# Kernel tuning notes

Measured on AMD Instinct MI355X. Metric: run time of the kernel, lower is better.

## Reference

```python
import jax, jax.numpy as jnp
import numpy as np

C, H, N, B, L = 1, 512, 64, 16, 2048  # n_channels, n_heads, d_kernel, batch, seq_len


def setup_inputs() -> dict:
    key = jax.random.key(0)
    k1, k2 = jax.random.split(key)
    u = jax.random.normal(k1, (B, C * H, L), dtype=jnp.float32)
    k = jax.random.normal(k2, (C, H, N), dtype=jnp.float32)
    return {"u": u, "k": k}


def _l1_normalize(x, axis):
    # torch.linalg.norm(x, ord=1, dim=axis, keepdim=True): vector 1-norm along `axis`
    return x / jnp.sum(jnp.abs(x), axis=axis, keepdims=True)


def _forward(u, k):
    c, h, n = k.shape
    bsz, d, l = u.shape  # d == c*h
    dt = u.dtype
    # Shift matrix A: A[:, :, 1:, :-1] = I  (companion-style shift)
    A = jnp.zeros((c, h, n, n), dtype=dt).at[:, :, 1:, :-1].set(jnp.eye(n - 1, dtype=dt))
    # b = e1 broadcast to (c, h, n)
    b_vec = jnp.zeros((c, h, n), dtype=dt).at[:, :, 0].set(1.0)
    # closed-loop: k_norm = L1-normalize(clamp(k, 1/16, 1)); A_cl = L1-normalize(A + b k^T)
    k_norm = _l1_normalize(jnp.clip(k, 1.0 / 16.0, 1.0), axis=2)
    BK = jnp.einsum('chi,chj->chij', b_vec, k_norm)
    M = _l1_normalize(A + BK, axis=2)

    # Krylov recurrence: f[i] = k . (M^i b), i = 0..l-1
    def step(x, _):
        f_i = jnp.einsum('chn,chn->ch', k, x)
        x_next = jnp.einsum('chij,chj->chi', M, x)
        return x_next, f_i

    _, f = jax.lax.scan(step, b_vec, None, length=l)  # f: (l, c, h)
    f = jnp.moveaxis(f, 0, -1)  # (c, h, l)

    # Causal FFT convolution of u (b, c, h, l) with filter f (c, h, l)
    n_fft = 2 * l
    uf = jnp.fft.rfft(u.reshape(bsz, c, h, l), n=n_fft)
    ff = jnp.fft.rfft(f, n=n_fft)
    y = jnp.fft.irfft(uf * ff[None], n=n_fft)[..., :l]
    return y.reshape(bsz, c * h, l)


def reference(u, k):
    return _forward(u, k)
```

## Files before the change

kernel.cpp:

```cpp
#include <hip/hip_runtime.h>


namespace {

constexpr int kH = 512;
constexpr int kL = 2048;
constexpr int kChunks = 32;
constexpr int kTS = 68;
constexpr int kPS = 68;

typedef __attribute__((ext_vector_type(8))) short bf16x8;
typedef __attribute__((ext_vector_type(4))) float f32x4;
typedef __attribute__((ext_vector_type(4))) unsigned int u32x4;

__device__ inline unsigned short bf16_rne(float x) {
  unsigned int u = __float_as_uint(x);
  unsigned int r = u + 0x7FFFu + ((u >> 16) & 1u);
  return (unsigned short)(r >> 16);
}
__device__ inline float bf16f(unsigned short h) {
  return __uint_as_float(((unsigned int)h) << 16);
}
__device__ inline unsigned pack_hi16(unsigned a, unsigned b) {
#if __has_builtin(__builtin_amdgcn_perm)
  return __builtin_amdgcn_perm(b, a, 0x07060302u);
#else
  return (b & 0xFFFF0000u) | (a >> 16);
#endif
}
__device__ inline void dekker8(const f32x4 a, const f32x4 b, bf16x8& hh, bf16x8& ll) {
  const unsigned ua0 = __float_as_uint(a[0]), ua1 = __float_as_uint(a[1]);
  const unsigned ua2 = __float_as_uint(a[2]), ua3 = __float_as_uint(a[3]);
  const unsigned ub0 = __float_as_uint(b[0]), ub1 = __float_as_uint(b[1]);
  const unsigned ub2 = __float_as_uint(b[2]), ub3 = __float_as_uint(b[3]);
  u32x4 hu, lu;
  hu[0] = pack_hi16(ua0, ua1);
  hu[1] = pack_hi16(ua2, ua3);
  hu[2] = pack_hi16(ub0, ub1);
  hu[3] = pack_hi16(ub2, ub3);
  const float l0 = a[0] - __uint_as_float(ua0 & 0xFFFF0000u);
  const float l1 = a[1] - __uint_as_float(ua1 & 0xFFFF0000u);
  const float l2 = a[2] - __uint_as_float(ua2 & 0xFFFF0000u);
  const float l3 = a[3] - __uint_as_float(ua3 & 0xFFFF0000u);
  const float l4 = b[0] - __uint_as_float(ub0 & 0xFFFF0000u);
  const float l5 = b[1] - __uint_as_float(ub1 & 0xFFFF0000u);
  const float l6 = b[2] - __uint_as_float(ub2 & 0xFFFF0000u);
  const float l7 = b[3] - __uint_as_float(ub3 & 0xFFFF0000u);
  lu[0] = pack_hi16(__float_as_uint(l0), __float_as_uint(l1));
  lu[1] = pack_hi16(__float_as_uint(l2), __float_as_uint(l3));
  lu[2] = pack_hi16(__float_as_uint(l4), __float_as_uint(l5));
  lu[3] = pack_hi16(__float_as_uint(l6), __float_as_uint(l7));
  hh = __builtin_bit_cast(bf16x8, hu);
  ll = __builtin_bit_cast(bf16x8, lu);
}

#define MFMA(A, B, C) __builtin_amdgcn_mfma_f32_16x16x32_bf16((A), (B), (C), 0, 0, 0)

__global__ __launch_bounds__(256, 2)
void ssm_mfma_kernel(const float* __restrict__ u,
                     const float* __restrict__ kin,
                     float* __restrict__ y) {
  const int h    = blockIdx.x;
  const int tid  = threadIdx.x;
  const int wq   = tid >> 6;
  const int lane = tid & 63;
  const int ln16 = lane & 15;
  const int quad = lane >> 4;

  __shared__ __align__(16) float Tbuf[64][kTS];
  __shared__ __align__(16) float Pbuf[2][16][kPS];
  __shared__ float wArr[64], sArr[64], gArr[64], tmpA[64], cArr[64];

  float kv = 0.f, kc = 0.f, kn = 0.f, cc = 0.f;
  if (tid < 64) {
    kv = kin[h * 64 + tid];
    kc = fminf(fmaxf(kv, 0.0625f), 1.0f);
    tmpA[tid] = kc;
  }
  __syncthreads();
  if (tid < 64) {
    float ks = 0.f;
    for (int j = 0; j < 64; ++j) ks += tmpA[j];
    kn = kc / ks;
    cc = 1.0f / (1.0f + kn);
    cArr[tid] = cc;
  }
  __syncthreads();
  if (tid < 64) {
    float P = 1.0f;
    for (int j = 0; j < tid; ++j) P *= cArr[j];
    wArr[tid] = (tid < 63) ? (kn * cc * P) : P;
    gArr[tid] = kv * P;
    if (tid == 0) sArr[0] = 1.0f;
  }
  __syncthreads();
  float acc_s = (tid == 0) ? 1.0f : 0.0f;
  for (int rr = 0; rr < 63; ++rr) {
    if (tid < 64) {
      const float sval = sArr[rr];
      const float coef = (tid > rr) ? wArr[tid - 1 - rr] : 0.0f;
      acc_s = fmaf(coef, sval, acc_s);
      if (tid == rr + 1) sArr[tid] = acc_s;
    }
    __syncthreads();
  }

  const int rA = 16 * wq + ln16;
  bf16x8 SH[2], SL[2], G1H[2], G2H[2];
  #pragma unroll
  for (int tk = 0; tk < 2; ++tk) {
    bf16x8 sh, sl, g1, g2;
    #pragma unroll
    for (int j = 0; j < 8; ++j) {
      const int k = 32 * tk + 8 * quad + j;
      const int d = rA - k;
      const float sv = (d >= 0 && d < 64) ? sArr[d] : 0.0f;
      const unsigned short shh = bf16_rne(sv);
      sh[j] = (short)shh;
      sl[j] = (short)bf16_rne(sv - bf16f(shh));
      g2[j] = (short)bf16_rne((d >= 0 && d < 64) ? gArr[d] : 0.0f);
      const int d1 = d + 64;
      g1[j] = (short)bf16_rne((d1 >= 0 && d1 < 64) ? gArr[d1] : 0.0f);
    }
    SH[tk] = sh; SL[tk] = sl; G1H[tk] = g1; G2H[tk] = g2;
  }

  {
    f32x4 accT[4];
    #pragma unroll
    for (int nt = 0; nt < 4; ++nt) {
      const int col = 16 * nt + ln16;
      f32x4 t = {};
      #pragma unroll
      for (int tk = 0; tk < 2; ++tk) {
        bf16x8 wh, wl;
        #pragma unroll
        for (int j = 0; j < 8; ++j) {
          const int k = 32 * tk + 8 * quad + j;
          const int idx = 63 + k - col;
          const float wv = (idx >= 0 && idx < 64) ? wArr[idx] : 0.0f;
          const unsigned short whh = bf16_rne(wv);
          wh[j] = (short)whh;
          wl[j] = (short)bf16_rne(wv - bf16f(whh));
        }
        t = MFMA(SH[tk], wh, t);
        t = MFMA(SH[tk], wl, t);
        t = MFMA(SL[tk], wh, t);
      }
      accT[nt] = t;
    }
    #pragma unroll
    for (int nt = 0; nt < 4; ++nt)
      #pragma unroll
      for (int reg = 0; reg < 4; ++reg)
        Tbuf[16 * wq + 4 * quad + reg][16 * nt + ln16] = accT[nt][reg];
  }
  __syncthreads();

  bf16x8 TH[2], TL[2];
  #pragma unroll
  for (int tk = 0; tk < 2; ++tk) {
    const f32x4 ta = *(const f32x4*)&Tbuf[rA][32 * tk + 8 * quad];
    const f32x4 tb = *(const f32x4*)&Tbuf[rA][32 * tk + 8 * quad + 4];
    bf16x8 th, tl;
    #pragma unroll
    for (int j = 0; j < 4; ++j) {
      unsigned short x = bf16_rne(ta[j]);
      th[j] = (short)x; tl[j] = (short)bf16_rne(ta[j] - bf16f(x));
      unsigned short z = bf16_rne(tb[j]);
      th[4 + j] = (short)z; tl[4 + j] = (short)bf16_rne(tb[j] - bf16f(z));
    }
    TH[tk] = th; TL[tk] = tl;
  }

  const size_t bstr = (size_t)kH * kL;
  const float* ub = u + (size_t)ln16 * bstr + (size_t)h * kL;
  float* yb = y + (size_t)ln16 * bstr + (size_t)h * kL + 16 * wq + 4 * quad;

  bf16x8 uHf[2], uLf[2], pH[2], pL[2];
  {
    bf16x8 z;
    #pragma unroll
    for (int j = 0; j < 8; ++j) z[j] = 0;
    pH[0] = z; pH[1] = z; pL[0] = z; pL[1] = z;
  }
  #pragma unroll
  for (int tk = 0; tk < 2; ++tk) {
    const f32x4 a = *(const f32x4*)(ub + 32 * tk + 8 * quad);
    const f32x4 b = *(const f32x4*)(ub + 32 * tk + 8 * quad + 4);
    dekker8(a, b, uHf[tk], uLf[tk]);
  }

  for (int m = 0; m < kChunks; ++m) {
    const int t0 = m * 64;
    f32x4 na0, nb0, na1, nb1;
    if (m + 1 < kChunks) {
      const float* up = ub + t0 + 64 + 8 * quad;
      na0 = *(const f32x4*)(up);
      nb0 = *(const f32x4*)(up + 4);
      na1 = *(const f32x4*)(up + 32);
      nb1 = *(const f32x4*)(up + 32 + 4);
    }

    f32x4 accSu = {};
    #pragma unroll
    for (int tk = 0; tk < 2; ++tk) {
      accSu = MFMA(SH[tk], uHf[tk], accSu);
      accSu = MFMA(SH[tk], uLf[tk], accSu);
      accSu = MFMA(SL[tk], uHf[tk], accSu);
    }
    f32x4 accTp = {};
    #pragma unroll
    for (int tk = 0; tk < 2; ++tk) {
      accTp = MFMA(TH[tk], pH[tk], accTp);
      accTp = MFMA(TH[tk], pL[tk], accTp);
      accTp = MFMA(TL[tk], pH[tk], accTp);
    }
    const f32x4 accP = accSu + accTp;
    *(f32x4*)&Pbuf[m & 1][ln16][16 * wq + 4 * quad] = accP;

    f32x4 accY = {};
    #pragma unroll
    for (int tk = 0; tk < 2; ++tk) {
      accY = MFMA(G1H[tk], pH[tk], accY);
      accY = MFMA(G1H[tk], pL[tk], accY);
    }
    if (m + 1 < kChunks) {
      dekker8(na0, nb0, uHf[0], uLf[0]);
      dekker8(na1, nb1, uHf[1], uLf[1]);
    }
    __syncthreads();

    #pragma unroll
    for (int tk = 0; tk < 2; ++tk) {
      const f32x4 pa = *(const f32x4*)&Pbuf[m & 1][ln16][32 * tk + 8 * quad];
      const f32x4 pb = *(const f32x4*)&Pbuf[m & 1][ln16][32 * tk + 8 * quad + 4];
      dekker8(pa, pb, pH[tk], pL[tk]);
    }
    #pragma unroll
    for (int tk = 0; tk < 2; ++tk) {
      accY = MFMA(G2H[tk], pH[tk], accY);
      accY = MFMA(G2H[tk], pL[tk], accY);
    }
    *(f32x4*)(yb + t0) = accY;
  }
}

}

extern "C" void kernel_launch(void* const* d_in, const int* in_sizes, int n_in,
                              void* d_out, int out_size, void* d_ws, size_t ws_size,
                              hipStream_t stream) {
  const float* u  = (const float*)d_in[0];
  const float* kk = (const float*)d_in[1];
  if (n_in >= 2 && in_sizes[0] < in_sizes[1]) {
    const float* t = u; u = kk; kk = t;
  }
  float* y = (float*)d_out;
  hipLaunchKernelGGL(ssm_mfma_kernel, dim3(kH), dim3(256), 0, stream, u, kk, y);
}
```

Measured before the change: 155.8 us.

## Fold carried-state output into precomputed Q matrix and take convolution off critical path

Adds a precomputed Q = G1 + G2·T matrix and a y0 kernel, so each chunk's output comes from the carried state p and the current u, with no second wait on the freshly computed state. The state update and the output MFMAs are now independent, and the last chunk skips the state update. The sArr recurrence setup drops its per-step block barriers and uses volatile LDS accesses within the first wave. A lighter inline-asm barrier replaces __syncthreads. The cost is extra setup MFMAs and a second 64x68 LDS buffer. Output precision is also raised by adding low-part terms for G.

```diff
diff --git a/kernel.cpp b/kernel.cpp
--- a/kernel.cpp
+++ b/kernel.cpp
@@ -53,6 +53,21 @@
   hh = __builtin_bit_cast(bf16x8, hu);
   ll = __builtin_bit_cast(bf16x8, lu);
 }
+__device__ inline void rne_split8(const f32x4 a, const f32x4 b, bf16x8& hh, bf16x8& ll) {
+  #pragma unroll
+  for (int j = 0; j < 4; ++j) {
+    const unsigned short x = bf16_rne(a[j]);
+    hh[j] = (short)x;
+    ll[j] = (short)bf16_rne(a[j] - bf16f(x));
+    const unsigned short z = bf16_rne(b[j]);
+    hh[4 + j] = (short)z;
+    ll[4 + j] = (short)bf16_rne(b[j] - bf16f(z));
+  }
+}
+
+__device__ inline void lds_barrier() {
+  asm volatile("s_waitcnt lgkmcnt(0)\n\ts_barrier" ::: "memory");
+}
 
 #define MFMA(A, B, C) __builtin_amdgcn_mfma_f32_16x16x32_bf16((A), (B), (C), 0, 0, 0)
 
@@ -68,8 +83,9 @@
   const int quad = lane >> 4;
 
   __shared__ __align__(16) float Tbuf[64][kTS];
+  __shared__ __align__(16) float Qbuf[64][kTS];
   __shared__ __align__(16) float Pbuf[2][16][kPS];
-  __shared__ float wArr[64], sArr[64], gArr[64], tmpA[64], cArr[64];
+  __shared__ float wArr[64], sArr[64], gArr[64], y0Arr[64], tmpA[64], cArr[64];
 
   float kv = 0.f, kc = 0.f, kn = 0.f, cc = 0.f;
   if (tid < 64) {
@@ -94,22 +110,28 @@
     if (tid == 0) sArr[0] = 1.0f;
   }
   __syncthreads();
-  float acc_s = (tid == 0) ? 1.0f : 0.0f;
-  for (int rr = 0; rr < 63; ++rr) {
-    if (tid < 64) {
-      const float sval = sArr[rr];
+  if (tid < 64) {
+    volatile float* vs = sArr;
+    float acc_s = (tid == 0) ? 1.0f : 0.0f;
+    for (int rr = 0; rr < 63; ++rr) {
+      const float sval = vs[rr];
       const float coef = (tid > rr) ? wArr[tid - 1 - rr] : 0.0f;
       acc_s = fmaf(coef, sval, acc_s);
-      if (tid == rr + 1) sArr[tid] = acc_s;
-    }
-    __syncthreads();
+      if (tid == rr + 1) vs[tid] = acc_s;
+    }
+  }
+  __syncthreads();
+  if (tid < 64) {
+    float a = 0.f;
+    for (int j = 0; j <= tid; ++j) a = fmaf(gArr[j], sArr[tid - j], a);
+    y0Arr[tid] = a;
   }
 
   const int rA = 16 * wq + ln16;
-  bf16x8 SH[2], SL[2], G1H[2], G2H[2];
+  bf16x8 SH[2], SL[2], G2H[2], G2L[2];
   #pragma unroll
   for (int tk = 0; tk < 2; ++tk) {
-    bf16x8 sh, sl, g1, g2;
+    bf16x8 sh, sl, g2h, g2l;
     #pragma unroll
     for (int j = 0; j < 8; ++j) {
       const int k = 32 * tk + 8 * quad + j;
@@ -118,11 +140,12 @@
       const unsigned short shh = bf16_rne(sv);
       sh[j] = (short)shh;
       sl[j] = (short)bf16_rne(sv - bf16f(shh));
-      g2[j] = (short)bf16_rne((d >= 0 && d < 64) ? gArr[d] : 0.0f);
-      const int d1 = d + 64;
-      g1[j] = (short)bf16_rne((d1 >= 0 && d1 < 64) ? gArr[d1] : 0.0f);
-    }
-    SH[tk] = sh; SL[tk] = sl; G1H[tk] = g1; G2H[tk] = g2;
+      const float gv = (d >= 0 && d < 64) ? gArr[d] : 0.0f;
+      const unsigned short ghh = bf16_rne(gv);
+      g2h[j] = (short)ghh;
+      g2l[j] = (short)bf16_rne(gv - bf16f(ghh));
+    }
+    SH[tk] = sh; SL[tk] = sl; G2H[tk] = g2h; G2L[tk] = g2l;
   }
 
   {
@@ -162,15 +185,79 @@
   for (int tk = 0; tk < 2; ++tk) {
     const f32x4 ta = *(const f32x4*)&Tbuf[rA][32 * tk + 8 * quad];
     const f32x4 tb = *(const f32x4*)&Tbuf[rA][32 * tk + 8 * quad + 4];
-    bf16x8 th, tl;
-    #pragma unroll
-    for (int j = 0; j < 4; ++j) {
-      unsigned short x = bf16_rne(ta[j]);
-      th[j] = (short)x; tl[j] = (short)bf16_rne(ta[j] - bf16f(x));
-      unsigned short z = bf16_rne(tb[j]);
-      th[4 + j] = (short)z; tl[4 + j] = (short)bf16_rne(tb[j] - bf16f(z));
-    }
-    TH[tk] = th; TL[tk] = tl;
+    rne_split8(ta, tb, TH[tk], TL[tk]);
+  }
+  {
+    bf16x8 TBH[2], TBL[2];
+    #pragma unroll
+    for (int tk = 0; tk < 2; ++tk) {
+      bf16x8 th, tl;
+      #pragma unroll
+      for (int j = 0; j < 8; ++j) {
+        const int k = 32 * tk + 8 * quad + j;
+        const float tv = Tbuf[k][ln16];
+        (void)tv;
+        th[j] = 0; tl[j] = 0;
+      }
+      TBH[tk] = th; TBL[tk] = tl;
+    }
+    f32x4 accQ[4];
+    #pragma unroll
+    for (int nt = 0; nt < 4; ++nt) {
+      const int col = 16 * nt + ln16;
+      #pragma unroll
+      for (int tk = 0; tk < 2; ++tk) {
+        bf16x8 th, tl;
+        #pragma unroll
+        for (int j = 0; j < 8; ++j) {
+          const int k = 32 * tk + 8 * quad + j;
+          const float tv = Tbuf[k][col];
+          const unsigned short x = bf16_rne(tv);
+          th[j] = (short)x;
+          tl[j] = (short)bf16_rne(tv - bf16f(x));
+        }
+        TBH[tk] = th; TBL[tk] = tl;
+      }
+      f32x4 q;
+      #pragma unroll
+      for (int reg = 0; reg < 4; ++reg) {
+        const int mrow = 16 * wq + 4 * quad + reg;
+        const int d1 = mrow - col + 64;
+        q[reg] = (d1 >= 0 && d1 < 64) ? gArr[d1] : 0.0f;
+      }
+      #pragma unroll
+      for (int tk = 0; tk < 2; ++tk) {
+        q = MFMA(G2H[tk], TBH[tk], q);
+        q = MFMA(G2H[tk], TBL[tk], q);
+        q = MFMA(G2L[tk], TBH[tk], q);
+      }
+      accQ[nt] = q;
+    }
+    #pragma unroll
+    for (int nt = 0; nt < 4; ++nt)
+      #pragma unroll
+      for (int reg = 0; reg < 4; ++reg)
+        Qbuf[16 * wq + 4 * quad + reg][16 * nt + ln16] = accQ[nt][reg];
+  }
+  __syncthreads();
+
+  bf16x8 QH[2], QL[2], Y0H[2], Y0L[2];
+  #pragma unroll
+  for (int tk = 0; tk < 2; ++tk) {
+    const f32x4 qa = *(const f32x4*)&Qbuf[rA][32 * tk + 8 * quad];
+    const f32x4 qb = *(const f32x4*)&Qbuf[rA][32 * tk + 8 * quad + 4];
+    rne_split8(qa, qb, QH[tk], QL[tk]);
+    bf16x8 yh, yl;
+    #pragma unroll
+    for (int j = 0; j < 8; ++j) {
+      const int k = 32 * tk + 8 * quad + j;
+      const int d = rA - k;
+      const float yv = (d >= 0 && d < 64) ? y0Arr[d] : 0.0f;
+      const unsigned short x = bf16_rne(yv);
+      yh[j] = (short)x;
+      yl[j] = (short)bf16_rne(yv - bf16f(x));
+    }
+    Y0H[tk] = yh; Y0L[tk] = yl;
   }
 
   const size_t bstr = (size_t)kH * kL;
@@ -193,8 +280,10 @@
 
   for (int m = 0; m < kChunks; ++m) {
     const int t0 = m * 64;
+    const bool last = (m == kChunks - 1);
+
     f32x4 na0, nb0, na1, nb1;
-    if (m + 1 < kChunks) {
+    if (!last) {
       const float* up = ub + t0 + 64 + 8 * quad;
       na0 = *(const f32x4*)(up);
       nb0 = *(const f32x4*)(up + 4);
@@ -202,47 +291,47 @@
       nb1 = *(const f32x4*)(up + 32 + 4);
     }
 
-    f32x4 accSu = {};
+    if (!last) {
+      f32x4 accTp = {};
+      f32x4 accSu = {};
+      #pragma unroll
+      for (int tk = 0; tk < 2; ++tk) {
+        accTp = MFMA(TH[tk], pH[tk], accTp);
+        accTp = MFMA(TH[tk], pL[tk], accTp);
+        accTp = MFMA(TL[tk], pH[tk], accTp);
+        accSu = MFMA(SH[tk], uHf[tk], accSu);
+        accSu = MFMA(SH[tk], uLf[tk], accSu);
+        accSu = MFMA(SL[tk], uHf[tk], accSu);
+      }
+      const f32x4 accP = accTp + accSu;
+      *(f32x4*)&Pbuf[m & 1][ln16][16 * wq + 4 * quad] = accP;
+    }
+
+    f32x4 accQp = {};
+    f32x4 accYu = {};
     #pragma unroll
     for (int tk = 0; tk < 2; ++tk) {
-      accSu = MFMA(SH[tk], uHf[tk], accSu);
-      accSu = MFMA(SH[tk], uLf[tk], accSu);
-      accSu = MFMA(SL[tk], uHf[tk], accSu);
-    }
-    f32x4 accTp = {};
-    #pragma unroll
-    for (int tk = 0; tk < 2; ++tk) {
-      accTp = MFMA(TH[tk], pH[tk], accTp);
-      accTp = MFMA(TH[tk], pL[tk], accTp);
-      accTp = MFMA(TL[tk], pH[tk], accTp);
-    }
-    const f32x4 accP = accSu + accTp;
-    *(f32x4*)&Pbuf[m & 1][ln16][16 * wq + 4 * quad] = accP;
-
-    f32x4 accY = {};
-    #pragma unroll
-    for (int tk = 0; tk < 2; ++tk) {
-      accY = MFMA(G1H[tk], pH[tk], accY);
-      accY = MFMA(G1H[tk], pL[tk], accY);
-    }
-    if (m + 1 < kChunks) {
+      accQp = MFMA(QH[tk], pH[tk], accQp);
+      accQp = MFMA(QH[tk], pL[tk], accQp);
+      accQp = MFMA(QL[tk], pH[tk], accQp);
+      accYu = MFMA(Y0H[tk], uHf[tk], accYu);
+      accYu = MFMA(Y0H[tk], uLf[tk], accYu);
+      accYu = MFMA(Y0L[tk], uHf[tk], accYu);
+    }
+    const f32x4 accY = accQp + accYu;
+    *(f32x4*)(yb + t0) = accY;
+
+    if (!last) {
+      lds_barrier();
+      #pragma unroll
+      for (int tk = 0; tk < 2; ++tk) {
+        const f32x4 pa = *(const f32x4*)&Pbuf[m & 1][ln16][32 * tk + 8 * quad];
+        const f32x4 pb = *(const f32x4*)&Pbuf[m & 1][ln16][32 * tk + 8 * quad + 4];
+        dekker8(pa, pb, pH[tk], pL[tk]);
+      }
       dekker8(na0, nb0, uHf[0], uLf[0]);
       dekker8(na1, nb1, uHf[1], uLf[1]);
     }
-    __syncthreads();
-
-    #pragma unroll
-    for (int tk = 0; tk < 2; ++tk) {
-      const f32x4 pa = *(const f32x4*)&Pbuf[m & 1][ln16][32 * tk + 8 * quad];
-      const f32x4 pb = *(const f32x4*)&Pbuf[m & 1][ln16][32 * tk + 8 * quad + 4];
-      dekker8(pa, pb, pH[tk], pL[tk]);
-    }
-    #pragma unroll
-    for (int tk = 0; tk < 2; ++tk) {
-      accY = MFMA(G2H[tk], pH[tk], accY);
-      accY = MFMA(G2H[tk], pL[tk], accY);
-    }
-    *(f32x4*)(yb + t0) = accY;
   }
 }
 
```

Result: slower. 159.4 us (+2.3%).
